# Performance work log

Hardware: AMD Instinct MI355X
Metric: run time of the kernel (lower is better)

Reference implementation:

```python
import jax, jax.numpy as jnp
import numpy as np

TEMPERATURE = 8.0  # sqrt(d_k), d_k = 64

def masked_softmax(x, m, axis):
    # Faithful to IBM/commonsense-rl masked_softmax:
    # clamp -> multiply by mask -> stable exp -> re-mask -> normalize (+1e-6)
    x = jnp.clip(x, -15.0, 15.0)
    m = m.astype(x.dtype)
    x = x * m
    e_x = jnp.exp(x - jnp.max(x, axis=axis, keepdims=True))
    e_x = e_x * m
    return e_x / (jnp.sum(e_x, axis=axis, keepdims=True) + 1e-6)

def setup_inputs() -> dict:
    key = jax.random.key(0)
    kq, kk, kv, km = jax.random.split(key, 4)
    B, Lq, Lk, d = 16, 2048, 2048, 64
    q = jax.random.normal(kq, (B, Lq, d), dtype=jnp.float32)
    k = jax.random.normal(kk, (B, Lk, d), dtype=jnp.float32)
    v = jax.random.normal(kv, (B, Lk, d), dtype=jnp.float32)
    mask = jax.random.randint(km, (B, Lq, Lk), 0, 2, dtype=jnp.int32)
    return {"q": q, "k": k, "v": v, "mask": mask}

def reference(q, k, v, mask):
    # attn scores: [B, Lq, Lk]
    attn = jnp.einsum('bqd,bkd->bqk', q, k) / TEMPERATURE
    attn = masked_softmax(attn, mask, axis=2)
    # dropout=0.0 (eval / deterministic reference): identity
    output = jnp.einsum('bqk,bkd->bqd', attn, v)
    return (output, attn)
```

## Files before the change

### kernel.cpp

```cpp
#include <hip/hip_runtime.h>
#include <hip/hip_bf16.h>
#include <math.h>


typedef __bf16 bf16x8v __attribute__((ext_vector_type(8)));
typedef __bf16 bf16x4v __attribute__((ext_vector_type(4)));
typedef __bf16 bf16x2v __attribute__((ext_vector_type(2)));
typedef float  f32x4   __attribute__((ext_vector_type(4)));
typedef int    i32x4   __attribute__((ext_vector_type(4)));

#define B_  16
#define L_  2048
#define D_  64
#define NKC 32

__device__ __forceinline__ int swz(int row, int colb) {
    return (row * 128 + colb) ^ ((row & 7) << 4);
}
__device__ __forceinline__ int swzF(int row, int colb) {
    return row * 256 + (colb ^ ((row & 7) << 4));
}

__device__ __forceinline__ void bar() {
    asm volatile("s_waitcnt lgkmcnt(0)" ::: "memory");
    __builtin_amdgcn_s_barrier();
}

__global__ __launch_bounds__(256, 2)
void sdpa_kernel(const float* __restrict__ qg,
                 const float* __restrict__ kg,
                 const float* __restrict__ vg,
                 const int*   __restrict__ mg,
                 float* __restrict__ outg,
                 float* __restrict__ attng)
{
    __shared__ __align__(16) char KtB[2][8192];
    __shared__ __align__(16) char VtB[2][8192];
    __shared__ __align__(16) char PwB[4][2048];
    __shared__ __align__(16) char PfB[4][4096];
    __shared__ unsigned short Ml[NKC][256];
    __shared__ unsigned Mn32[4][64];

    const int t  = threadIdx.x;
    const int w  = t >> 6;
    const int l  = t & 63;
    const int lq = l & 15;
    const int g  = l >> 4;

    const int bid  = blockIdx.x;
    const int virt = (bid & 7) * 64 + (bid >> 3);
    const int b  = virt >> 5;
    const int q0 = (virt & 31) * 64;
    const int qi = q0 + w * 16 + lq;

    const size_t kvbase = (size_t)b * (L_ * D_);
    const size_t mrow   = ((size_t)b * L_ + qi) * L_;
    const size_t qwrow  = (size_t)b * L_ + q0 + w * 16;

    bf16x8v qf0, qf1;
    {
        const float* qrow = qg + ((size_t)b * L_ + qi) * D_;
        const f32x4* p0 = (const f32x4*)(qrow + g * 8);
        const f32x4* p1 = (const f32x4*)(qrow + 32 + g * 8);
        f32x4 x0 = p0[0], x1 = p0[1], x2 = p1[0], x3 = p1[1];
        #pragma unroll
        for (int j = 0; j < 4; ++j) {
            qf0[j]     = (__bf16)(x0[j] * 0.125f);
            qf0[4 + j] = (__bf16)(x1[j] * 0.125f);
            qf1[j]     = (__bf16)(x2[j] * 0.125f);
            qf1[4 + j] = (__bf16)(x3[j] * 0.125f);
        }
    }

    const int sr  = t >> 2;
    const int scb = (t & 3) * 32;
    const float* kbase  = kg + kvbase + (size_t)sr * D_ + (t & 3) * 16;
    const float* vbase0 = vg + kvbase + (size_t)(2 * (t & 31)) * D_ + (t >> 5) * 8;
    const int dg = t >> 5, kp = t & 31;
    const int* mbase = mg + (qwrow + (l >> 4)) * L_ + (l & 15) * 4;

    auto loadK = [&](int kc, f32x4& a, f32x4& bb, f32x4& c, f32x4& d) {
        const f32x4* s = (const f32x4*)(kbase + (size_t)kc * (64 * D_));
        a = s[0]; bb = s[1]; c = s[2]; d = s[3];
    };
    auto writeK = [&](char* buf, f32x4 a, f32x4 bb, f32x4 c, f32x4 d) {
        bf16x8v h0, h1;
        #pragma unroll
        for (int j = 0; j < 4; ++j) {
            h0[j] = (__bf16)a[j]; h0[4 + j] = (__bf16)bb[j];
            h1[j] = (__bf16)c[j]; h1[4 + j] = (__bf16)d[j];
        }
        *(bf16x8v*)(buf + swz(sr, scb))      = h0;
        *(bf16x8v*)(buf + swz(sr, scb + 16)) = h1;
    };
    auto loadV = [&](int kc, f32x4& a, f32x4& bb, f32x4& c, f32x4& d) {
        const float* r0 = vbase0 + (size_t)kc * (64 * D_);
        const f32x4* s0 = (const f32x4*)r0;
        const f32x4* s1 = (const f32x4*)(r0 + D_);
        a = s0[0]; bb = s0[1]; c = s1[0]; d = s1[1];
    };
    auto writeV = [&](char* buf, f32x4 a, f32x4 bb, f32x4 c, f32x4 d) {
        #pragma unroll
        for (int j = 0; j < 4; ++j) {
            bf16x2v p0; p0[0] = (__bf16)a[j];  p0[1] = (__bf16)c[j];
            *(bf16x2v*)(buf + swz(dg * 8 + j, kp * 4)) = p0;
            bf16x2v p1; p1[0] = (__bf16)bb[j]; p1[1] = (__bf16)d[j];
            *(bf16x2v*)(buf + swz(dg * 8 + 4 + j, kp * 4)) = p1;
        }
    };
    auto loadM = [&](int kc, i32x4& m0, i32x4& m1, i32x4& m2, i32x4& m3) {
        const int* p = mbase + kc * 64;
        m0 = *(const i32x4*)(p);
        m1 = *(const i32x4*)(p + 4 * L_);
        m2 = *(const i32x4*)(p + 8 * L_);
        m3 = *(const i32x4*)(p + 12 * L_);
    };

    float rS = 0.f;
    float inv = 0.f;

    auto compute1 = [&](const char* KB, int kc, i32x4 m0, i32x4 m1, i32x4 m2, i32x4 m3) {
        auto nib = [](i32x4 m) -> unsigned {
            return (m[0] ? 1u : 0u) | (m[1] ? 2u : 0u) | (m[2] ? 4u : 0u) | (m[3] ? 8u : 0u);
        };
        Mn32[w][l] = nib(m0) | (nib(m1) << 8) | (nib(m2) << 16) | (nib(m3) << 24);
        asm volatile("s_waitcnt lgkmcnt(0)" ::: "memory");
        unsigned mbits = 0;
        const int sh = (lq >> 2) * 8;
        #pragma unroll
        for (int sub = 0; sub < 4; ++sub) {
            unsigned nb = (Mn32[w][(lq & 3) * 16 + sub * 4 + g] >> sh) & 0xFu;
            mbits |= nb << (sub * 4);
        }
        float part = 0.f;
        #pragma unroll
        for (int sub = 0; sub < 4; ++sub) {
            bf16x8v a0 = *(const bf16x8v*)(KB + swz(sub * 16 + lq, g * 16));
            bf16x8v a1 = *(const bf16x8v*)(KB + swz(sub * 16 + lq, 64 + g * 16));
            f32x4 s = {0.f, 0.f, 0.f, 0.f};
            s = __builtin_amdgcn_mfma_f32_16x16x32_bf16(a0, qf0, s, 0, 0, 0);
            s = __builtin_amdgcn_mfma_f32_16x16x32_bf16(a1, qf1, s, 0, 0, 0);
            #pragma unroll
            for (int r = 0; r < 4; ++r) {
                bool mm = (mbits >> (sub * 4 + r)) & 1u;
                float y = mm ? (fminf(fmaxf(s[r], -15.f), 15.f) - 15.f) : -1e30f;
                part += __expf(y);
            }
        }
        rS += part;
        Ml[kc][t] = (unsigned short)mbits;
    };

    f32x4 acc[4];
    #pragma unroll
    for (int i = 0; i < 4; ++i) acc[i] = (f32x4){0.f, 0.f, 0.f, 0.f};

    auto compute2 = [&](const char* KB, const char* VB, int kc) {
        const unsigned mbits = Ml[kc][t];
        char* PFw = PfB[w];
        #pragma unroll
        for (int sub = 0; sub < 4; ++sub) {
            bf16x8v a0 = *(const bf16x8v*)(KB + swz(sub * 16 + lq, g * 16));
            bf16x8v a1 = *(const bf16x8v*)(KB + swz(sub * 16 + lq, 64 + g * 16));
            f32x4 s = {0.f, 0.f, 0.f, 0.f};
            s = __builtin_amdgcn_mfma_f32_16x16x32_bf16(a0, qf0, s, 0, 0, 0);
            s = __builtin_amdgcn_mfma_f32_16x16x32_bf16(a1, qf1, s, 0, 0, 0);
            f32x4 pv; bf16x4v pb;
            #pragma unroll
            for (int r = 0; r < 4; ++r) {
                bool mm = (mbits >> (sub * 4 + r)) & 1u;
                float y = mm ? (fminf(fmaxf(s[r], -15.f), 15.f) - 15.f) : -1e30f;
                float p = __expf(y) * inv;
                pv[r] = p; pb[r] = (__bf16)p;
            }
            *(f32x4*)(PFw + swzF(lq, (sub * 16 + g * 4) * 4)) = pv;
            *(bf16x4v*)(PwB[w] + swz(lq, (sub * 16 + g * 4) * 2)) = pb;
        }
        #pragma unroll
        for (int ks = 0; ks < 2; ++ks) {
            bf16x8v pa = *(const bf16x8v*)(PwB[w] + swz(lq, ks * 64 + g * 16));
            #pragma unroll
            for (int dt = 0; dt < 4; ++dt) {
                bf16x8v vb = *(const bf16x8v*)(VB + swz(dt * 16 + lq, ks * 64 + g * 16));
                acc[dt] = __builtin_amdgcn_mfma_f32_16x16x32_bf16(pa, vb, acc[dt], 0, 0, 0);
            }
        }
        #pragma unroll
        for (int j = 0; j < 4; ++j) {
            const int row = (l >> 4) + 4 * j;
            const int col = (l & 15) * 4;
            f32x4 o = *(const f32x4*)(PFw + swzF(row, col * 4));
            *(f32x4*)(attng + (qwrow + row) * L_ + kc * 64 + col) = o;
        }
    };

    f32x4 kA0, kA1, kA2, kA3, kB0, kB1, kB2, kB3;
    f32x4 vA0, vA1, vA2, vA3, vB0, vB1, vB2, vB3;
    i32x4 mA0, mA1, mA2, mA3, mB0, mB1, mB2, mB3;

    loadK(0, kA0, kA1, kA2, kA3);
    loadM(0, mA0, mA1, mA2, mA3);
    writeK(KtB[0], kA0, kA1, kA2, kA3);
    loadK(1, kB0, kB1, kB2, kB3);
    loadM(1, mB0, mB1, mB2, mB3);
    bar();
    #pragma unroll 1
    for (int kc = 0; kc < NKC; kc += 2) {
        { int kn = (kc + 2 < NKC) ? kc + 2 : NKC - 1; loadK(kn, kA0, kA1, kA2, kA3); }
        compute1(KtB[0], kc, mA0, mA1, mA2, mA3);
        { int kn = (kc + 2 < NKC) ? kc + 2 : NKC - 1; loadM(kn, mA0, mA1, mA2, mA3); }
        writeK(KtB[1], kB0, kB1, kB2, kB3);
        bar();
        { int kn = (kc + 3 < NKC) ? kc + 3 : NKC - 1; loadK(kn, kB0, kB1, kB2, kB3); }
        compute1(KtB[1], kc + 1, mB0, mB1, mB2, mB3);
        { int kn = (kc + 3 < NKC) ? kc + 3 : NKC - 1; loadM(kn, mB0, mB1, mB2, mB3); }
        writeK(KtB[0], kA0, kA1, kA2, kA3);
        bar();
    }

    loadK(0, kA0, kA1, kA2, kA3);
    loadV(0, vA0, vA1, vA2, vA3);
    rS += __shfl_xor(rS, 16, 64);
    rS += __shfl_xor(rS, 32, 64);
    inv = 1.f / (rS + 1e-6f);

    writeK(KtB[0], kA0, kA1, kA2, kA3);
    writeV(VtB[0], vA0, vA1, vA2, vA3);
    loadK(1, kB0, kB1, kB2, kB3);
    loadV(1, vB0, vB1, vB2, vB3);
    bar();
    #pragma unroll 1
    for (int kc = 0; kc < NKC; kc += 2) {
        { int kn = (kc + 2 < NKC) ? kc + 2 : NKC - 1;
          loadK(kn, kA0, kA1, kA2, kA3); loadV(kn, vA0, vA1, vA2, vA3); }
        compute2(KtB[0], VtB[0], kc);
        writeK(KtB[1], kB0, kB1, kB2, kB3);
        writeV(VtB[1], vB0, vB1, vB2, vB3);
        bar();
        { int kn = (kc + 3 < NKC) ? kc + 3 : NKC - 1;
          loadK(kn, kB0, kB1, kB2, kB3); loadV(kn, vB0, vB1, vB2, vB3); }
        compute2(KtB[1], VtB[1], kc + 1);
        writeK(KtB[0], kA0, kA1, kA2, kA3);
        writeV(VtB[0], vA0, vA1, vA2, vA3);
        bar();
    }

    #pragma unroll
    for (int dt = 0; dt < 4; ++dt) {
        #pragma unroll
        for (int r = 0; r < 4; ++r) {
            outg[((size_t)b * L_ + (q0 + w * 16 + g * 4 + r)) * D_ + dt * 16 + lq] = acc[dt][r];
        }
    }
}

extern "C" void kernel_launch(void* const* d_in, const int* in_sizes, int n_in,
                              void* d_out, int out_size, void* d_ws, size_t ws_size,
                              hipStream_t stream) {
    (void)in_sizes; (void)n_in; (void)out_size; (void)d_ws; (void)ws_size;
    const float* q = (const float*)d_in[0];
    const float* k = (const float*)d_in[1];
    const float* v = (const float*)d_in[2];
    const int*   m = (const int*)d_in[3];
    float* out  = (float*)d_out;
    float* attn = out + (size_t)B_ * L_ * D_;
    dim3 grid(B_ * (L_ / 64));
    dim3 block(256);
    hipLaunchKernelGGL(sdpa_kernel, grid, block, 0, stream, q, k, v, m, out, attn);
}
```

Before: 176.1 us.

## Split key chunks across wave pairs with 32-row blocks and global mask-bit workspace

Each block now covers 32 query rows, and the two waves of each pair split the key chunks by parity. Both K (and V) chunks are staged in shared memory per step, and row sums and output partials are combined through LDS at the end. The fp32 P staging buffer and the LDS mask tables are removed, so the attn output is now written by widening the bf16 P values. Mask bits are exchanged with shuffles and spilled to a global workspace for the second pass. The goal is to cut LDS use and raise occupancy (launch bounds 4) and grid size, at the cost of extra barriers and a loss of precision in the stored attn values.

```diff
diff --git a/kernel.cpp b/kernel.cpp
--- a/kernel.cpp
+++ b/kernel.cpp
@@ -9,53 +9,50 @@
 typedef float  f32x4   __attribute__((ext_vector_type(4)));
 typedef int    i32x4   __attribute__((ext_vector_type(4)));
 
-#define B_  16
-#define L_  2048
-#define D_  64
-#define NKC 32
+#define B_    16
+#define L_    2048
+#define D_    64
+#define NKC   32
+#define NPAIR 16
 
 __device__ __forceinline__ int swz(int row, int colb) {
     return (row * 128 + colb) ^ ((row & 7) << 4);
 }
-__device__ __forceinline__ int swzF(int row, int colb) {
-    return row * 256 + (colb ^ ((row & 7) << 4));
-}
-
 __device__ __forceinline__ void bar() {
     asm volatile("s_waitcnt lgkmcnt(0)" ::: "memory");
     __builtin_amdgcn_s_barrier();
 }
 
-__global__ __launch_bounds__(256, 2)
+template<bool UB>
+__global__ __launch_bounds__(256, 4)
 void sdpa_kernel(const float* __restrict__ qg,
                  const float* __restrict__ kg,
                  const float* __restrict__ vg,
                  const int*   __restrict__ mg,
+                 unsigned short* __restrict__ bitws,
                  float* __restrict__ outg,
                  float* __restrict__ attng)
 {
     __shared__ __align__(16) char KtB[2][8192];
     __shared__ __align__(16) char VtB[2][8192];
     __shared__ __align__(16) char PwB[4][2048];
-    __shared__ __align__(16) char PfB[4][4096];
-    __shared__ unsigned short Ml[NKC][256];
-    __shared__ unsigned Mn32[4][64];
 
     const int t  = threadIdx.x;
     const int w  = t >> 6;
     const int l  = t & 63;
     const int lq = l & 15;
     const int g  = l >> 4;
+    const int pair = w >> 1;
+    const int par  = w & 1;
 
     const int bid  = blockIdx.x;
-    const int virt = (bid & 7) * 64 + (bid >> 3);
-    const int b  = virt >> 5;
-    const int q0 = (virt & 31) * 64;
-    const int qi = q0 + w * 16 + lq;
+    const int virt = (bid & 7) * 128 + (bid >> 3);
+    const int b    = virt >> 6;
+    const int q0   = (virt & 63) * 32;
+    const int qi   = q0 + pair * 16 + lq;
 
     const size_t kvbase = (size_t)b * (L_ * D_);
-    const size_t mrow   = ((size_t)b * L_ + qi) * L_;
-    const size_t qwrow  = (size_t)b * L_ + q0 + w * 16;
+    const size_t qwrow  = (size_t)b * L_ + q0 + pair * 16;
 
     bf16x8v qf0, qf1;
     {
@@ -79,59 +76,75 @@
     const int dg = t >> 5, kp = t & 31;
     const int* mbase = mg + (qwrow + (l >> 4)) * L_ + (l & 15) * 4;
 
-    auto loadK = [&](int kc, f32x4& a, f32x4& bb, f32x4& c, f32x4& d) {
+    f32x4 kE[4], kO[4], vE[4], vO[4];
+    i32x4 mA[4], mB[4];
+    unsigned bitA = 0, bitB = 0;
+
+    auto loadKt = [&](int kc, f32x4* r) {
         const f32x4* s = (const f32x4*)(kbase + (size_t)kc * (64 * D_));
-        a = s[0]; bb = s[1]; c = s[2]; d = s[3];
-    };
-    auto writeK = [&](char* buf, f32x4 a, f32x4 bb, f32x4 c, f32x4 d) {
+        #pragma unroll
+        for (int j = 0; j < 4; ++j) r[j] = s[j];
+    };
+    auto writeKt = [&](char* buf, const f32x4* r) {
         bf16x8v h0, h1;
         #pragma unroll
         for (int j = 0; j < 4; ++j) {
-            h0[j] = (__bf16)a[j]; h0[4 + j] = (__bf16)bb[j];
-            h1[j] = (__bf16)c[j]; h1[4 + j] = (__bf16)d[j];
+            h0[j] = (__bf16)r[0][j]; h0[4 + j] = (__bf16)r[1][j];
+            h1[j] = (__bf16)r[2][j]; h1[4 + j] = (__bf16)r[3][j];
         }
         *(bf16x8v*)(buf + swz(sr, scb))      = h0;
         *(bf16x8v*)(buf + swz(sr, scb + 16)) = h1;
     };
-    auto loadV = [&](int kc, f32x4& a, f32x4& bb, f32x4& c, f32x4& d) {
+    auto loadVt = [&](int kc, f32x4* r) {
         const float* r0 = vbase0 + (size_t)kc * (64 * D_);
         const f32x4* s0 = (const f32x4*)r0;
         const f32x4* s1 = (const f32x4*)(r0 + D_);
-        a = s0[0]; bb = s0[1]; c = s1[0]; d = s1[1];
-    };
-    auto writeV = [&](char* buf, f32x4 a, f32x4 bb, f32x4 c, f32x4 d) {
+        r[0] = s0[0]; r[1] = s0[1]; r[2] = s1[0]; r[3] = s1[1];
+    };
+    auto writeVt = [&](char* buf, const f32x4* r) {
         #pragma unroll
         for (int j = 0; j < 4; ++j) {
-            bf16x2v p0; p0[0] = (__bf16)a[j];  p0[1] = (__bf16)c[j];
+            bf16x2v p0; p0[0] = (__bf16)r[0][j]; p0[1] = (__bf16)r[2][j];
             *(bf16x2v*)(buf + swz(dg * 8 + j, kp * 4)) = p0;
-            bf16x2v p1; p1[0] = (__bf16)bb[j]; p1[1] = (__bf16)d[j];
+            bf16x2v p1; p1[0] = (__bf16)r[1][j]; p1[1] = (__bf16)r[3][j];
             *(bf16x2v*)(buf + swz(dg * 8 + 4 + j, kp * 4)) = p1;
         }
     };
-    auto loadM = [&](int kc, i32x4& m0, i32x4& m1, i32x4& m2, i32x4& m3) {
+    auto loadM = [&](int kc, i32x4* m) {
         const int* p = mbase + kc * 64;
-        m0 = *(const i32x4*)(p);
-        m1 = *(const i32x4*)(p + 4 * L_);
-        m2 = *(const i32x4*)(p + 8 * L_);
-        m3 = *(const i32x4*)(p + 12 * L_);
+        m[0] = *(const i32x4*)(p);
+        m[1] = *(const i32x4*)(p + 4 * L_);
+        m[2] = *(const i32x4*)(p + 8 * L_);
+        m[3] = *(const i32x4*)(p + 12 * L_);
+    };
+    auto xchg = [&](const i32x4* m) -> unsigned {
+        auto nib = [](i32x4 v) -> unsigned {
+            return (v[0] ? 1u : 0u) | (v[1] ? 2u : 0u) | (v[2] ? 4u : 0u) | (v[3] ? 8u : 0u);
+        };
+        unsigned packed = nib(m[0]) | (nib(m[1]) << 8) | (nib(m[2]) << 16) | (nib(m[3]) << 24);
+        const int sh = (lq >> 2) * 8;
+        unsigned mb = 0;
+        #pragma unroll
+        for (int sub = 0; sub < 4; ++sub) {
+            unsigned v = (unsigned)__shfl((int)packed, (lq & 3) * 16 + sub * 4 + g, 64);
+            mb |= ((v >> sh) & 0xFu) << (sub * 4);
+        }
+        return mb;
+    };
+
+    auto pcK = [&](int p) { return p < NPAIR ? p : NPAIR - 1; };
+    auto mt  = [&](int p) { int v = 2 * p + par, mx = 2 * (NPAIR - 1) + par;
+                            return v < mx ? v : mx; };
+    auto bidx = [&](int kc) -> size_t {
+        return ((size_t)virt * NKC + kc) * 128 + pair * 64 + l;
     };
 
     float rS = 0.f;
     float inv = 0.f;
 
-    auto compute1 = [&](const char* KB, int kc, i32x4 m0, i32x4 m1, i32x4 m2, i32x4 m3) {
-        auto nib = [](i32x4 m) -> unsigned {
-            return (m[0] ? 1u : 0u) | (m[1] ? 2u : 0u) | (m[2] ? 4u : 0u) | (m[3] ? 8u : 0u);
-        };
-        Mn32[w][l] = nib(m0) | (nib(m1) << 8) | (nib(m2) << 16) | (nib(m3) << 24);
-        asm volatile("s_waitcnt lgkmcnt(0)" ::: "memory");
-        unsigned mbits = 0;
-        const int sh = (lq >> 2) * 8;
-        #pragma unroll
-        for (int sub = 0; sub < 4; ++sub) {
-            unsigned nb = (Mn32[w][(lq & 3) * 16 + sub * 4 + g] >> sh) & 0xFu;
-            mbits |= nb << (sub * 4);
-        }
+    auto compute1 = [&](int kc, unsigned mbits) {
+        const char* KB = KtB[par];
+        if (UB) bitws[bidx(kc)] = (unsigned short)mbits;
         float part = 0.f;
         #pragma unroll
         for (int sub = 0; sub < 4; ++sub) {
@@ -148,16 +161,15 @@
             }
         }
         rS += part;
-        Ml[kc][t] = (unsigned short)mbits;
     };
 
     f32x4 acc[4];
     #pragma unroll
     for (int i = 0; i < 4; ++i) acc[i] = (f32x4){0.f, 0.f, 0.f, 0.f};
 
-    auto compute2 = [&](const char* KB, const char* VB, int kc) {
-        const unsigned mbits = Ml[kc][t];
-        char* PFw = PfB[w];
+    auto compute2 = [&](int kc, unsigned mbits) {
+        const char* KB = KtB[par];
+        const char* VB = VtB[par];
         #pragma unroll
         for (int sub = 0; sub < 4; ++sub) {
             bf16x8v a0 = *(const bf16x8v*)(KB + swz(sub * 16 + lq, g * 16));
@@ -165,15 +177,13 @@
             f32x4 s = {0.f, 0.f, 0.f, 0.f};
             s = __builtin_amdgcn_mfma_f32_16x16x32_bf16(a0, qf0, s, 0, 0, 0);
             s = __builtin_amdgcn_mfma_f32_16x16x32_bf16(a1, qf1, s, 0, 0, 0);
-            f32x4 pv; bf16x4v pb;
+            bf16x4v pb;
             #pragma unroll
             for (int r = 0; r < 4; ++r) {
                 bool mm = (mbits >> (sub * 4 + r)) & 1u;
                 float y = mm ? (fminf(fmaxf(s[r], -15.f), 15.f) - 15.f) : -1e30f;
-                float p = __expf(y) * inv;
-                pv[r] = p; pb[r] = (__bf16)p;
+                pb[r] = (__bf16)(__expf(y) * inv);
             }
-            *(f32x4*)(PFw + swzF(lq, (sub * 16 + g * 4) * 4)) = pv;
             *(bf16x4v*)(PwB[w] + swz(lq, (sub * 16 + g * 4) * 2)) = pb;
         }
         #pragma unroll
@@ -189,82 +199,116 @@
         for (int j = 0; j < 4; ++j) {
             const int row = (l >> 4) + 4 * j;
             const int col = (l & 15) * 4;
-            f32x4 o = *(const f32x4*)(PFw + swzF(row, col * 4));
+            bf16x4v pq = *(const bf16x4v*)(PwB[w] + swz(row, col * 2));
+            f32x4 o;
+            #pragma unroll
+            for (int c = 0; c < 4; ++c) o[c] = (float)pq[c];
             *(f32x4*)(attng + (qwrow + row) * L_ + kc * 64 + col) = o;
         }
     };
 
-    f32x4 kA0, kA1, kA2, kA3, kB0, kB1, kB2, kB3;
-    f32x4 vA0, vA1, vA2, vA3, vB0, vB1, vB2, vB3;
-    i32x4 mA0, mA1, mA2, mA3, mB0, mB1, mB2, mB3;
-
-    loadK(0, kA0, kA1, kA2, kA3);
-    loadM(0, mA0, mA1, mA2, mA3);
-    writeK(KtB[0], kA0, kA1, kA2, kA3);
-    loadK(1, kB0, kB1, kB2, kB3);
-    loadM(1, mB0, mB1, mB2, mB3);
+    loadKt(0, kE); loadKt(1, kO);
+    loadM(mt(0), mA);
+    writeKt(KtB[0], kE); writeKt(KtB[1], kO);
+    loadM(mt(1), mB);
+    loadKt(2, kE); loadKt(3, kO);
     bar();
     #pragma unroll 1
-    for (int kc = 0; kc < NKC; kc += 2) {
-        { int kn = (kc + 2 < NKC) ? kc + 2 : NKC - 1; loadK(kn, kA0, kA1, kA2, kA3); }
-        compute1(KtB[0], kc, mA0, mA1, mA2, mA3);
-        { int kn = (kc + 2 < NKC) ? kc + 2 : NKC - 1; loadM(kn, mA0, mA1, mA2, mA3); }
-        writeK(KtB[1], kB0, kB1, kB2, kB3);
-        bar();
-        { int kn = (kc + 3 < NKC) ? kc + 3 : NKC - 1; loadK(kn, kB0, kB1, kB2, kB3); }
-        compute1(KtB[1], kc + 1, mB0, mB1, mB2, mB3);
-        { int kn = (kc + 3 < NKC) ? kc + 3 : NKC - 1; loadM(kn, mB0, mB1, mB2, mB3); }
-        writeK(KtB[0], kA0, kA1, kA2, kA3);
-        bar();
-    }
-
-    loadK(0, kA0, kA1, kA2, kA3);
-    loadV(0, vA0, vA1, vA2, vA3);
+    for (int i = 0; i < NPAIR; i += 2) {
+        compute1(2 * i + par, xchg(mA));
+        bar();
+        writeKt(KtB[0], kE); writeKt(KtB[1], kO);
+        loadKt(2 * pcK(i + 2), kE); loadKt(2 * pcK(i + 2) + 1, kO);
+        loadM(mt(i + 2), mA);
+        bar();
+        compute1(2 * (i + 1) + par, xchg(mB));
+        bar();
+        writeKt(KtB[0], kE); writeKt(KtB[1], kO);
+        loadKt(2 * pcK(i + 3), kE); loadKt(2 * pcK(i + 3) + 1, kO);
+        loadM(mt(i + 3), mB);
+        bar();
+    }
+
     rS += __shfl_xor(rS, 16, 64);
     rS += __shfl_xor(rS, 32, 64);
-    inv = 1.f / (rS + 1e-6f);
-
-    writeK(KtB[0], kA0, kA1, kA2, kA3);
-    writeV(VtB[0], vA0, vA1, vA2, vA3);
-    loadK(1, kB0, kB1, kB2, kB3);
-    loadV(1, vB0, vB1, vB2, vB3);
+    asm volatile("s_waitcnt vmcnt(0)" ::: "memory");
+    {
+        float* sx = (float*)(PwB[0]);
+        if (l < 16) sx[w * 16 + l] = rS;
+        bar();
+        float oth = sx[(pair * 2 + (1 - par)) * 16 + lq];
+        inv = 1.f / (rS + oth + 1e-6f);
+        bar();
+    }
+
+    loadKt(0, kE); loadKt(1, kO);
+    loadVt(0, vE); loadVt(1, vO);
+    if (UB) bitA = bitws[bidx(mt(0))]; else loadM(mt(0), mA);
+    writeKt(KtB[0], kE); writeKt(KtB[1], kO);
+    writeVt(VtB[0], vE); writeVt(VtB[1], vO);
+    if (UB) bitB = bitws[bidx(mt(1))]; else loadM(mt(1), mB);
+    loadKt(2, kE); loadKt(3, kO);
+    loadVt(2, vE); loadVt(3, vO);
     bar();
     #pragma unroll 1
-    for (int kc = 0; kc < NKC; kc += 2) {
-        { int kn = (kc + 2 < NKC) ? kc + 2 : NKC - 1;
-          loadK(kn, kA0, kA1, kA2, kA3); loadV(kn, vA0, vA1, vA2, vA3); }
-        compute2(KtB[0], VtB[0], kc);
-        writeK(KtB[1], kB0, kB1, kB2, kB3);
-        writeV(VtB[1], vB0, vB1, vB2, vB3);
-        bar();
-        { int kn = (kc + 3 < NKC) ? kc + 3 : NKC - 1;
-          loadK(kn, kB0, kB1, kB2, kB3); loadV(kn, vB0, vB1, vB2, vB3); }
-        compute2(KtB[1], VtB[1], kc + 1);
-        writeK(KtB[0], kA0, kA1, kA2, kA3);
-        writeV(VtB[0], vA0, vA1, vA2, vA3);
-        bar();
-    }
-
-    #pragma unroll
-    for (int dt = 0; dt < 4; ++dt) {
-        #pragma unroll
-        for (int r = 0; r < 4; ++r) {
-            outg[((size_t)b * L_ + (q0 + w * 16 + g * 4 + r)) * D_ + dt * 16 + lq] = acc[dt][r];
-        }
+    for (int i = 0; i < NPAIR; i += 2) {
+        compute2(2 * i + par, UB ? bitA : xchg(mA));
+        bar();
+        writeKt(KtB[0], kE); writeKt(KtB[1], kO);
+        writeVt(VtB[0], vE); writeVt(VtB[1], vO);
+        loadKt(2 * pcK(i + 2), kE); loadKt(2 * pcK(i + 2) + 1, kO);
+        loadVt(2 * pcK(i + 2), vE); loadVt(2 * pcK(i + 2) + 1, vO);
+        if (UB) bitA = bitws[bidx(mt(i + 2))]; else loadM(mt(i + 2), mA);
+        bar();
+        compute2(2 * (i + 1) + par, UB ? bitB : xchg(mB));
+        bar();
+        writeKt(KtB[0], kE); writeKt(KtB[1], kO);
+        writeVt(VtB[0], vE); writeVt(VtB[1], vO);
+        loadKt(2 * pcK(i + 3), kE); loadKt(2 * pcK(i + 3) + 1, kO);
+        loadVt(2 * pcK(i + 3), vE); loadVt(2 * pcK(i + 3) + 1, vO);
+        if (UB) bitB = bitws[bidx(mt(i + 3))]; else loadM(mt(i + 3), mB);
+        bar();
+    }
+
+    float* ob = (float*)(KtB[0]) + pair * 1088;
+    if (par == 1) {
+        #pragma unroll
+        for (int dt = 0; dt < 4; ++dt)
+            #pragma unroll
+            for (int r = 0; r < 4; ++r)
+                ob[(g * 4 + r) * 68 + dt * 16 + lq] = acc[dt][r];
+    }
+    bar();
+    if (par == 0) {
+        #pragma unroll
+        for (int dt = 0; dt < 4; ++dt)
+            #pragma unroll
+            for (int r = 0; r < 4; ++r) {
+                float o = acc[dt][r] + ob[(g * 4 + r) * 68 + dt * 16 + lq];
+                outg[(qwrow + g * 4 + r) * D_ + dt * 16 + lq] = o;
+            }
     }
 }
 
 extern "C" void kernel_launch(void* const* d_in, const int* in_sizes, int n_in,
                               void* d_out, int out_size, void* d_ws, size_t ws_size,
                               hipStream_t stream) {
-    (void)in_sizes; (void)n_in; (void)out_size; (void)d_ws; (void)ws_size;
+    (void)in_sizes; (void)n_in; (void)out_size;
     const float* q = (const float*)d_in[0];
     const float* k = (const float*)d_in[1];
     const float* v = (const float*)d_in[2];
     const int*   m = (const int*)d_in[3];
     float* out  = (float*)d_out;
     float* attn = out + (size_t)B_ * L_ * D_;
-    dim3 grid(B_ * (L_ / 64));
-    dim3 block(256);
-    hipLaunchKernelGGL(sdpa_kernel, grid, block, 0, stream, q, k, v, m, out, attn);
+    unsigned short* bitws = (unsigned short*)d_ws;
+    const size_t need = (size_t)1024 * NKC * 128 * sizeof(unsigned short);
+
+    dim3 grid(1024), block(256);
+    if (ws_size >= need) {
+        hipLaunchKernelGGL((sdpa_kernel<true>),  grid, block, 0, stream,
+                           q, k, v, m, bitws, out, attn);
+    } else {
+        hipLaunchKernelGGL((sdpa_kernel<false>), grid, block, 0, stream,
+                           q, k, v, m, (unsigned short*)nullptr, out, attn);
+    }
 }
```

Result: slower. 347.4 us (+97.2%).
